# Kernel tuning notes

Hardware: AMD Instinct MI355X
Metric: run time of the kernel (lower is better)

Reference implementation:

```python
import jax, jax.numpy as jnp
import numpy as np

B, T, Rn, D, O, E, H, C, TM = 20, 20, 20, 4096, 16, 512, 8, 68, 1900


def l2norm(x, axis=-1, eps=1e-12):
    return x / jnp.maximum(jnp.linalg.norm(x, axis=axis, keepdims=True), eps)


def setup_inputs() -> dict:
    key = jax.random.key(0)
    ks = jax.random.split(key, 10)
    return {
        "features": jax.random.normal(ks[0], (B, T, Rn, D), jnp.float32),
        "labels": jax.random.randint(ks[1], (B, O), 0, C),
        "temporal_mem": jax.random.normal(ks[2], (TM, T, D), jnp.float32),
        "entity_W": jax.random.normal(ks[3], (C, E), jnp.float32) / np.float32(np.sqrt(C)),
        "entity_b": jnp.zeros((E,), jnp.float32),
        "Wq": jax.random.normal(ks[4], (E, E), jnp.float32) / np.float32(np.sqrt(E)),
        "Wk": jax.random.normal(ks[5], (D, E), jnp.float32) / np.float32(np.sqrt(D)),
        "Wv": jax.random.normal(ks[6], (D, E), jnp.float32) / np.float32(np.sqrt(D)),
        "Wo": jax.random.normal(ks[7], (E, E), jnp.float32) / np.float32(np.sqrt(E)),
        "obj_W1": jax.random.normal(ks[8], (D, E), jnp.float32) / np.float32(np.sqrt(D)),
        "obj_b1": jnp.zeros((E,), jnp.float32),
        "obj_W2": jax.random.normal(ks[9], (E, 1), jnp.float32) / np.float32(np.sqrt(E)),
        "obj_b2": jnp.zeros((1,), jnp.float32),
    }


def reference(features, labels, temporal_mem, entity_W, entity_b, Wq, Wk, Wv, Wo,
              obj_W1, obj_b1, obj_W2, obj_b2):
    beta = 0.5   # loss mixing weight (module's beta)
    qgce = 0.7   # generalized-CE exponent
    Dh = E // H
    # region features, L2-normalized (dataset_feat == 'CVPR' path)
    Rf = l2norm(features)                                   # [B,T,Rn,D]

    # ---- temporal memory-bank kNN retrieval ----
    R_max = l2norm(jnp.max(Rf, axis=2))                     # [B,T,D] max-pool over regions
    mem_max = l2norm(jnp.max(temporal_mem, axis=1))         # [TM,D] max-pool over frames
    sim = jnp.einsum('btd,md->btm', R_max, mem_max)         # [B,T,TM]
    idx = jnp.argmax(sim, axis=-1)                          # [B,T] nearest memory slot
    Rp = temporal_mem[idx]                                  # [B,T,T,D] gathered memory videos
    mem_feat = jnp.max(Rp, axis=2)                          # [B,T,D]

    # ---- entity (object-label) embedding: one-hot with class 0 zeroed ----
    onehot = jax.nn.one_hot(labels, C, dtype=features.dtype)
    onehot = onehot * (labels != 0)[..., None].astype(features.dtype)
    Qe = onehot @ entity_W + entity_b                       # [B,O,E]

    # ---- multi-head attention fusion over regions + retrieved memory ----
    kv = jnp.concatenate([Rf.reshape(B, T * Rn, D), mem_feat], axis=1)  # [B,N,D]
    q = (Qe @ Wq).reshape(B, O, H, Dh)
    k = (kv @ Wk).reshape(B, -1, H, Dh)
    v = (kv @ Wv).reshape(B, -1, H, Dh)
    scores = jnp.einsum('bohd,bnhd->bhon', q, k) / np.float32(np.sqrt(Dh))
    attn = jax.nn.softmax(scores, axis=-1)
    fused = jnp.einsum('bhon,bnhd->bohd', attn, v).reshape(B, O, E) @ Wo  # [B,O,E]

    # ---- top-k region objectness selection + generalized CE ----
    QR = jax.lax.stop_gradient(jnp.mean(scores, axis=1)[:, :, :T * Rn].reshape(B, O, T, Rn))
    hi = jnp.argmax(QR, axis=-1)                            # [B,O,T] top-1 region
    lo = jnp.argmin(QR, axis=-1)                            # [B,O,T] low region
    bidx = jnp.arange(B)[:, None, None]
    tidx = jnp.arange(T)[None, None, :]
    R_high = Rf[bidx, tidx, hi]                             # [B,O,T,D]
    R_low = Rf[bidx, tidx, lo]                              # [B,O,T,D]
    osel = (labels != 0).astype(features.dtype)             # [B,O]
    onum = jnp.maximum(jnp.sum(osel, axis=1), 1.0)
    mlp = lambda x: jax.nn.sigmoid(jnp.tanh(x @ obj_W1 + obj_b1) @ obj_W2 + obj_b2)
    s_hi = mlp(R_high * osel[..., None, None]).squeeze(-1)  # [B,O,T]
    s_lo = mlp(R_low * osel[..., None, None]).squeeze(-1)
    gce_hi = jnp.mean((1.0 - (s_hi + 1e-7) ** qgce) / qgce * osel[..., None], axis=-1)
    gce_lo = jnp.mean((1.0 - (1.0 - s_lo + 1e-7) ** qgce) / qgce * osel[..., None], axis=-1)
    gce = jnp.mean(jnp.sum(gce_hi, axis=1) / onum) + jnp.mean(jnp.sum(gce_lo, axis=1) / onum)

    return fused + beta * gce
```

## Files before the change

kernel.cpp:

```cpp
#include <hip/hip_runtime.h>

#define B_   20
#define T_   20
#define RN   20
#define D_   4096
#define O_   16
#define E_   512
#define H_   8
#define DH   64
#define TM_  1900
#define MREG 8192
#define NW   1536
#define NSIM 2048
#define MSIM 512
#define CAP  256
#define NT32 128

using f32x4  = __attribute__((ext_vector_type(4))) float;
using bf16x8 = __attribute__((ext_vector_type(8))) __bf16;

__device__ __forceinline__ unsigned short f2bf(float f){
  unsigned u = __float_as_uint(f);
  u += 0x7fffu + ((u >> 16) & 1u);
  return (unsigned short)(u >> 16);
}

__device__ __forceinline__ void st_bf4(unsigned short* dst, float4 v){
  ushort4 o = make_ushort4(f2bf(v.x), f2bf(v.y), f2bf(v.z), f2bf(v.w));
  *(ushort4*)dst = o;
}

__device__ __forceinline__ float bsum256(float v, float* sh){
  int t = threadIdx.x;
  for (int o = 32; o; o >>= 1) v += __shfl_down(v, o, 64);
  __syncthreads();
  if ((t & 63) == 0) sh[t >> 6] = v;
  __syncthreads();
  return sh[0] + sh[1] + sh[2] + sh[3];
}

__device__ __forceinline__ float bmax256(float v, float* sh){
  int t = threadIdx.x;
  for (int o = 32; o; o >>= 1) v = fmaxf(v, __shfl_down(v, o, 64));
  __syncthreads();
  if ((t & 63) == 0) sh[t >> 6] = v;
  __syncthreads();
  return fmaxf(fmaxf(sh[0], sh[1]), fmaxf(sh[2], sh[3]));
}

__device__ __forceinline__ void gld16(const void* g, void* l){
  __builtin_amdgcn_global_load_lds(
      (const __attribute__((address_space(1))) unsigned int*)g,
      (__attribute__((address_space(3))) unsigned int*)l, 16, 0, 0);
}

__global__ __launch_bounds__(256) void k_pre(
    const float* __restrict__ F, const float* __restrict__ TMm,
    const float* __restrict__ Wk, const float* __restrict__ Wv, const float* __restrict__ W1,
    unsigned short* __restrict__ Wall,
    unsigned short* __restrict__ A, float* __restrict__ rmaxr, float* __restrict__ rmsum,
    unsigned short* __restrict__ ubf,
    float* __restrict__ umax, float* __restrict__ msum, unsigned short* __restrict__ wnorm,
    unsigned short* __restrict__ gbf,
    const int* __restrict__ labels, const float* __restrict__ entW, const float* __restrict__ entB,
    const float* __restrict__ Wq, float* __restrict__ q){
  __shared__ char smem[4352];
  int bid = blockIdx.x, t = threadIdx.x;
  if (bid < 2048){
    int m = bid;
    if (m >= TM_){
      int4 zz = make_int4(0,0,0,0);
      int4* r1 = (int4*)(wnorm + (size_t)m*D_);
      int4* r2 = (int4*)(gbf + (size_t)m*D_);
      r1[t] = zz; r1[t + 256] = zz;
      r2[t] = zz; r2[t + 256] = zz;
      return;
    }
    float* sh = (float*)smem;
    const float* base = TMm + (size_t)m*T_*D_;
    float4 mx[4];
#pragma unroll
    for (int i = 0; i < 4; ++i) mx[i] = make_float4(-1e30f,-1e30f,-1e30f,-1e30f);
    float4 va[2][4];
#pragma unroll
    for (int i = 0; i < 4; ++i) va[0][i] = *(const float4*)(base + i*1024 + t*4);
#pragma unroll
    for (int f = 0; f < T_; ++f){
      int c = f & 1;
      if (f + 1 < T_){
#pragma unroll
        for (int i = 0; i < 4; ++i)
          va[c^1][i] = *(const float4*)(base + (size_t)(f+1)*D_ + i*1024 + t*4);
      }
#pragma unroll
      for (int i = 0; i < 4; ++i){
        mx[i].x = fmaxf(mx[i].x, va[c][i].x); mx[i].y = fmaxf(mx[i].y, va[c][i].y);
        mx[i].z = fmaxf(mx[i].z, va[c][i].z); mx[i].w = fmaxf(mx[i].w, va[c][i].w);
      }
    }
    float s = 0.f;
#pragma unroll
    for (int i = 0; i < 4; ++i){
      *(float4*)(umax + (size_t)m*D_ + i*1024 + t*4) = mx[i];
      st_bf4(gbf + (size_t)m*D_ + i*1024 + t*4, mx[i]);
      s += mx[i].x*mx[i].x + mx[i].y*mx[i].y + mx[i].z*mx[i].z + mx[i].w*mx[i].w;
    }
    s = bsum256(s, sh);
    if (t == 0) msum[m] = s;
    float inv = 1.f / fmaxf(sqrtf(s), 1e-12f);
#pragma unroll
    for (int i = 0; i < 4; ++i){
      float4 u = mx[i];
      u.x *= inv; u.y *= inv; u.z *= inv; u.w *= inv;
      st_bf4(wnorm + (size_t)m*D_ + i*1024 + t*4, u);
    }
  } else if (bid < 2560){
    int bt = bid - 2048;
    if (bt >= 400){
      int4 zz = make_int4(0,0,0,0);
      int4* r1 = (int4*)(ubf + (size_t)bt*D_);
      r1[t] = zz; r1[t + 256] = zz;
      int base = 8000 + (bt - 400)*2;
#pragma unroll
      for (int k = 0; k < 2; ++k){
        if (base + k < MREG){
          int4* r2 = (int4*)(A + (size_t)(base + k)*D_);
          r2[t] = zz; r2[t + 256] = zz;
        }
      }
      return;
    }
    float* sh = (float*)smem;
    const float* fb = F + (size_t)bt*RN*D_;
    unsigned short* ab = A + (size_t)bt*RN*D_;
    float4 mx[4];
#pragma unroll
    for (int i = 0; i < 4; ++i) mx[i] = make_float4(-1e30f,-1e30f,-1e30f,-1e30f);
    float4 vn[4];
#pragma unroll
    for (int i = 0; i < 4; ++i) vn[i] = *(const float4*)(fb + i*1024 + t*4);
    for (int r = 0; r < RN; ++r){
      float4 v[4];
      float s = 0.f;
#pragma unroll
      for (int i = 0; i < 4; ++i){
        v[i] = vn[i];
        s += v[i].x*v[i].x + v[i].y*v[i].y + v[i].z*v[i].z + v[i].w*v[i].w;
      }
      if (r + 1 < RN){
#pragma unroll
        for (int i = 0; i < 4; ++i)
          vn[i] = *(const float4*)(fb + (size_t)(r+1)*D_ + i*1024 + t*4);
      }
      s = bsum256(s, sh);
      float ri = 1.f / fmaxf(sqrtf(s), 1e-12f);
#pragma unroll
      for (int i = 0; i < 4; ++i){
        v[i].x *= ri; v[i].y *= ri; v[i].z *= ri; v[i].w *= ri;
        st_bf4(ab + (size_t)r*D_ + i*1024 + t*4, v[i]);
        mx[i].x = fmaxf(mx[i].x, v[i].x); mx[i].y = fmaxf(mx[i].y, v[i].y);
        mx[i].z = fmaxf(mx[i].z, v[i].z); mx[i].w = fmaxf(mx[i].w, v[i].w);
      }
    }
    float s2 = 0.f;
#pragma unroll
    for (int i = 0; i < 4; ++i){
      *(float4*)(rmaxr + (size_t)bt*D_ + i*1024 + t*4) = mx[i];
      s2 += mx[i].x*mx[i].x + mx[i].y*mx[i].y + mx[i].z*mx[i].z + mx[i].w*mx[i].w;
    }
    s2 = bsum256(s2, sh);
    if (t == 0) rmsum[bt] = s2;
    float inv = 1.f / fmaxf(sqrtf(s2), 1e-12f);
#pragma unroll
    for (int i = 0; i < 4; ++i){
      float4 u = mx[i];
      u.x *= inv; u.y *= inv; u.z *= inv; u.w *= inv;
      st_bf4(ubf + (size_t)bt*D_ + i*1024 + t*4, u);
    }
  } else if (bid < 8704){
    int wti = bid - 2560;
    float* tile = (float*)smem;
    int kb = (wti & 127) * 32, nb = (wti >> 7) * 32;
    const float* src; int nc0;
    if (nb < 512)      { src = Wk; nc0 = nb; }
    else if (nb < 1024){ src = Wv; nc0 = nb - 512; }
    else               { src = W1; nc0 = nb - 1024; }
    int tx = t & 31, ty = t >> 5;
#pragma unroll
    for (int j = 0; j < 4; ++j){
      int k = kb + ty + j*8;
      tile[(ty + j*8)*33 + tx] = src[(size_t)k*E_ + nc0 + tx];
    }
    __syncthreads();
#pragma unroll
    for (int j = 0; j < 4; ++j){
      int n = nb + ty + j*8;
      int k = kb + tx;
      Wall[(size_t)n*D_ + k] = f2bf(tile[tx*33 + ty + j*8]);
    }
  } else {
    int bo = bid - 8704;
    float* qe = (float*)smem;
    int lab = labels[bo];
    float sel = (lab != 0) ? 1.f : 0.f;
    qe[t]       = sel * entW[(size_t)lab*E_ + t]       + entB[t];
    qe[t + 256] = sel * entW[(size_t)lab*E_ + t + 256] + entB[t + 256];
    __syncthreads();
    float a0 = 0.f, a1 = 0.f;
    for (int ep = 0; ep < E_; ++ep){
      float r = qe[ep];
      a0 += r * Wq[(size_t)ep*E_ + t];
      a1 += r * Wq[(size_t)ep*E_ + t + 256];
    }
    q[(size_t)bo*E_ + t] = a0;
    q[(size_t)bo*E_ + t + 256] = a1;
  }
}

__global__ __launch_bounds__(512, 1) void k_gemm3(
    const unsigned short* __restrict__ Akv, const unsigned short* __restrict__ Wall,
    const unsigned short* __restrict__ ubf, const unsigned short* __restrict__ wnorm,
    const unsigned short* __restrict__ gbf,
    float* __restrict__ C2, float* __restrict__ simc, float* __restrict__ Gc){
  __shared__ char lds[98304];
  int bid = blockIdx.x;
  bid = (bid & 7)*32 + (bid >> 3);
  const unsigned short *A, *Bw; float* C; int nNt, ldc, mt, nt;
  if (bid < 192){       A = Akv; Bw = Wall;  C = C2;   nNt = 6; ldc = NW;   mt = bid/6;  nt = bid%6; }
  else if (bid < 208){  int s = bid - 192;
                        A = ubf; Bw = wnorm; C = simc; nNt = 8; ldc = NSIM; mt = s/8;    nt = s%8; }
  else {                int s = bid - 208;
                        A = gbf; Bw = Wall;  C = Gc;   nNt = 6; ldc = NW;   mt = s/6;    nt = s%6; }
  int tid = threadIdx.x, wid = tid >> 6, l = tid & 63;
  int wr = (wid >> 2) * 128;
  int wc = (wid & 3) * 64;
  int fr = l & 15, fq = l >> 4;
  const char* Ab = (const char*)A + (size_t)mt*256*(size_t)(D_*2);
  const char* Bb = (const char*)Bw + (size_t)nt*256*(size_t)(D_*2);
  f32x4 acc[8][4];
#pragma unroll
  for (int m = 0; m < 8; ++m)
#pragma unroll
    for (int n = 0; n < 4; ++n) acc[m][n] = (f32x4){0.f,0.f,0.f,0.f};

  auto stage = [&](char* dst, int ktt){
    int ktoff = ktt * 64;
#pragma unroll
    for (int i = 0; i < 2; ++i){
      int s = i*512 + tid;
      int row = s >> 2, u = s & 3;
      int ul = u ^ (row & 3);
      gld16(Ab + (size_t)row*(D_*2) + ktoff + ul*16, dst + s*16);
      gld16(Bb + (size_t)row*(D_*2) + ktoff + ul*16, dst + 16384 + s*16);
    }
  };

  stage(lds, 0);
  stage(lds + 32768, 1);
  stage(lds + 65536, 2);

  int cur = 0;
  for (int kt = 0; kt < NT32; ++kt){
    if (kt < NT32 - 2)       asm volatile("s_waitcnt vmcnt(8)" ::: "memory");
    else if (kt == NT32 - 2) asm volatile("s_waitcnt vmcnt(4)" ::: "memory");
    else                     asm volatile("s_waitcnt vmcnt(0)" ::: "memory");
    __builtin_amdgcn_s_barrier();
    __builtin_amdgcn_sched_barrier(0);
    const char* LA = lds + cur*32768;
    const char* LB = LA + 16384;
    bf16x8 bv[4];
#pragma unroll
    for (int n = 0; n < 4; ++n){
      int row = wc + n*16 + fr;
      int u = fq ^ (row & 3);
      bv[n] = *(const bf16x8*)(LB + row*64 + u*16);
    }
    __builtin_amdgcn_s_setprio(1);
#pragma unroll
    for (int mp = 0; mp < 4; ++mp){
      bf16x8 av[2];
#pragma unroll
      for (int mm = 0; mm < 2; ++mm){
        int row = wr + (mp*2 + mm)*16 + fr;
        int u = fq ^ (row & 3);
        av[mm] = *(const bf16x8*)(LA + row*64 + u*16);
      }
#pragma unroll
      for (int mm = 0; mm < 2; ++mm)
#pragma unroll
        for (int n = 0; n < 4; ++n)
          acc[mp*2 + mm][n] = __builtin_amdgcn_mfma_f32_16x16x32_bf16(
              av[mm], bv[n], acc[mp*2 + mm][n], 0, 0, 0);
    }
    __builtin_amdgcn_s_setprio(0);
    __builtin_amdgcn_s_barrier();
    if (kt + 3 < NT32)
      stage(lds + cur*32768, kt + 3);
    cur = (cur == 2) ? 0 : cur + 1;
  }
  size_t crow0 = (size_t)mt*256 + wr, ccol0 = (size_t)nt*256 + wc;
#pragma unroll
  for (int m = 0; m < 8; ++m)
#pragma unroll
    for (int n = 0; n < 4; ++n){
      size_t r0 = crow0 + m*16 + fq*4, c0 = ccol0 + n*16 + fr;
#pragma unroll
      for (int j = 0; j < 4; ++j)
        C[(r0 + j)*(size_t)ldc + c0] = acc[m][n][j];
    }
}

__global__ __launch_bounds__(256) void k_pick(const float* __restrict__ simc,
                                              const float* __restrict__ rmaxr, const float* __restrict__ rmsum,
                                              const float* __restrict__ umax, const float* __restrict__ msum,
                                              const float* __restrict__ Gc, float* __restrict__ C2){
  int bt = blockIdx.x, t = threadIdx.x;
  __shared__ float srow[1920];
  __shared__ float sh[4];
  __shared__ int cnt;
  __shared__ int cl[CAP];
  for (int m = t; m < TM_; m += 256) srow[m] = simc[(size_t)bt*NSIM + m];
  if (t == 0) cnt = 0;
  __syncthreads();
  float mx = -1e30f;
  for (int m = t; m < TM_; m += 256) mx = fmaxf(mx, srow[m]);
  mx = bmax256(mx, sh);
  float thr = mx - 2.5e-4f;
  for (int m = t; m < TM_; m += 256){
    if (srow[m] >= thr){
      int p = atomicAdd(&cnt, 1);
      if (p < CAP) cl[p] = m;
    }
  }
  __syncthreads();
  int cn = cnt < CAP ? cnt : CAP;
  float rinvv = 1.f / fmaxf(sqrtf(rmsum[bt]), 1e-12f);
  const float* a = rmaxr + (size_t)bt*D_;
  float best = -1e30f; int bestm = 0x7fffffff;
  for (int ci = 0; ci < cn; ++ci){
    int m = cl[ci];
    const float* wrow = umax + (size_t)m*D_;
    float p = 0.f;
    for (int i = t*4; i < D_; i += 1024){
      float4 av = *(const float4*)(a + i);
      float4 wv = *(const float4*)(wrow + i);
      p += av.x*wv.x + av.y*wv.y + av.z*wv.z + av.w*wv.w;
    }
    p = bsum256(p, sh);
    float sim = p * rinvv * (1.f / fmaxf(sqrtf(msum[m]), 1e-12f));
    if (sim > best || (sim == best && m < bestm)){ best = sim; bestm = m; }
  }
  const float4* src = (const float4*)(Gc + (size_t)bestm*NW);
  float4* dst = (float4*)(C2 + (size_t)(MREG + bt)*NW);
  if (t < 128){ dst[t] = src[t]; dst[t + 128] = src[t + 128]; dst[t + 256] = src[t + 256]; }
}

__global__ __launch_bounds__(256) void k_post(const float* __restrict__ q, const float* __restrict__ c2,
                                              float* __restrict__ fpre, int* __restrict__ hi,
                                              int* __restrict__ lo, const float* __restrict__ b1,
                                              const float* __restrict__ W2, const float* __restrict__ b2,
                                              float* __restrict__ z){
  __shared__ char smem[58368];
  int bid = blockIdx.x, t = threadIdx.x;
  if (bid < 160){
    int b = bid >> 3, h = bid & 7;
    int w = t >> 6, l = t & 63;
    float* qhp = (float*)smem;
    float* kb  = (float*)(smem + 4160);
    float* sc  = (float*)(smem + 31460);
    for (int i = t; i < O_*DH; i += 256){
      int o = i >> 6, d = i & 63;
      qhp[o*65 + d] = q[((size_t)(b*O_ + o))*E_ + h*DH + d] * 0.125f;
    }
    __syncthreads();
    for (int c = 0; c < 4; ++c){
      for (int i = t; i < 105*DH; i += 256){
        int j = i >> 6, d = i & 63;
        int n = c*105 + j;
        size_t row = n < 400 ? (size_t)b*400 + n : (size_t)MREG + b*20 + (n - 400);
        kb[j*65 + d] = c2[row*NW + h*DH + d];
      }
      __syncthreads();
      for (int i = t; i < O_*105; i += 256){
        int o = i / 105, j = i % 105;
        float acc = 0.f;
        for (int d = 0; d < DH; ++d) acc += qhp[o*65 + d] * kb[j*65 + d];
        sc[o*420 + c*105 + j] = acc;
      }
      __syncthreads();
    }
    for (int oi = 0; oi < 4; ++oi){
      int o = w + oi*4;
      float mxv = -1e30f;
      for (int n = l; n < 420; n += 64) mxv = fmaxf(mxv, sc[o*420 + n]);
      for (int of = 32; of; of >>= 1) mxv = fmaxf(mxv, __shfl_xor(mxv, of, 64));
      float sum = 0.f;
      for (int n = l; n < 420; n += 64){ float e = expf(sc[o*420 + n] - mxv); sc[o*420 + n] = e; sum += e; }
      for (int of = 32; of; of >>= 1) sum += __shfl_xor(sum, of, 64);
      float inv = 1.f / sum;
      for (int n = l; n < 420; n += 64) sc[o*420 + n] *= inv;
    }
    __syncthreads();
    float acc[4] = {0.f, 0.f, 0.f, 0.f};
    for (int c = 0; c < 4; ++c){
      for (int i = t; i < 105*DH; i += 256){
        int j = i >> 6, d = i & 63;
        int n = c*105 + j;
        size_t row = n < 400 ? (size_t)b*400 + n : (size_t)MREG + b*20 + (n - 400);
        kb[j*65 + d] = c2[row*NW + E_ + h*DH + d];
      }
      __syncthreads();
#pragma unroll
      for (int og = 0; og < 4; ++og){
        int o = og*4 + w;
        float a = 0.f;
        for (int j = 0; j < 105; ++j) a += sc[o*420 + c*105 + j] * kb[j*65 + l];
        acc[og] += a;
      }
      __syncthreads();
    }
#pragma unroll
    for (int og = 0; og < 4; ++og){
      int o = og*4 + w;
      fpre[((size_t)(b*O_ + o))*E_ + h*DH + l] = acc[og];
    }
  } else if (bid < 560){
    int bt = bid - 160;
    int b = bt / T_, tt = bt % T_;
    float* kl = (float*)smem;
    float* qr = (float*)(smem + 41040);
    for (int i = t; i < RN*E_; i += 256){
      int r = i >> 9, e = i & 511;
      kl[r*513 + e] = c2[((size_t)b*400 + tt*RN + r)*NW + e];
    }
    __syncthreads();
#pragma unroll
    for (int pp = 0; pp < 2; ++pp){
      int p = t + pp*256;
      if (p < O_*RN){
        int o = p / RN, r = p % RN;
        const float* qrow = q + ((size_t)(b*O_ + o))*E_;
        float acc = 0.f;
        for (int e = 0; e < E_; ++e) acc += qrow[e] * kl[r*513 + e];
        qr[o*20 + r] = acc;
      }
    }
    __syncthreads();
    if (t < O_){
      int o = t;
      float bh = qr[o*20], bl = qr[o*20]; int ih = 0, il = 0;
#pragma unroll
      for (int r = 1; r < RN; ++r){
        float v = qr[o*20 + r];
        if (v > bh){ bh = v; ih = r; }
        if (v < bl){ bl = v; il = r; }
      }
      int rowbase = b*400 + tt*RN;
      int outi = (b*O_ + o)*T_ + tt;
      hi[outi] = rowbase + ih;
      lo[outi] = rowbase + il;
    }
  } else {
    int g = (bid - 560)*4 + (t >> 6);
    int l = t & 63;
    const float* hrow = c2 + (size_t)g*NW + 1024;
    float acc = 0.f;
    for (int e = l; e < E_; e += 64) acc += tanhf(hrow[e] + b1[e]) * W2[e];
    for (int of = 32; of; of >>= 1) acc += __shfl_down(acc, of, 64);
    if (l == 0) z[g] = 1.f / (1.f + expf(-(acc + b2[0])));
  }
}

__global__ __launch_bounds__(256) void k_outg(const float* __restrict__ fpre, const float* __restrict__ Wo,
                                              const float* __restrict__ z, const int* __restrict__ hi,
                                              const int* __restrict__ lo, const int* __restrict__ labels,
                                              float* __restrict__ out){
  int bo = blockIdx.x, t = threadIdx.x;
  __shared__ float rowv[E_];
  __shared__ float vb[B_];
  __shared__ int cb[B_];
  __shared__ float gsh;
  rowv[t] = fpre[(size_t)bo*E_ + t];
  rowv[t + 256] = fpre[(size_t)bo*E_ + t + 256];
  if (t < B_){ vb[t] = 0.f; cb[t] = 0; }
  __syncthreads();
  for (int p = t; p < B_*O_; p += 256){
    int b = p / O_;
    if (labels[p] != 0){
      float acc = 0.f;
      for (int tt = 0; tt < T_; ++tt){
        float shi = z[hi[p*T_ + tt]];
        float slo = z[lo[p*T_ + tt]];
        acc += (1.f - __powf(shi + 1e-7f, 0.7f)) / 0.7f;
        acc += (1.f - __powf(1.f - slo + 1e-7f, 0.7f)) / 0.7f;
      }
      atomicAdd(&vb[b], acc / (float)T_);
      atomicAdd(&cb[b], 1);
    }
  }
  __syncthreads();
  if (t == 0){
    float g = 0.f;
    for (int b = 0; b < B_; ++b) g += vb[b] / fmaxf((float)cb[b], 1.f);
    gsh = 0.5f * (g / (float)B_);
  }
  __syncthreads();
  float g = gsh;
  float a0 = 0.f, a1 = 0.f;
  for (int ep = 0; ep < E_; ++ep){
    float r = rowv[ep];
    a0 += r * Wo[(size_t)ep*E_ + t];
    a1 += r * Wo[(size_t)ep*E_ + t + 256];
  }
  out[(size_t)bo*E_ + t] = a0 + g;
  out[(size_t)bo*E_ + t + 256] = a1 + g;
}

extern "C" void kernel_launch(void* const* d_in, const int* in_sizes, int n_in,
                              void* d_out, int out_size, void* d_ws, size_t ws_size,
                              hipStream_t stream) {
  (void)in_sizes; (void)n_in; (void)out_size; (void)ws_size;
  const float* F    = (const float*)d_in[0];
  const int*   labels = (const int*)d_in[1];
  const float* TMm  = (const float*)d_in[2];
  const float* entW = (const float*)d_in[3];
  const float* entB = (const float*)d_in[4];
  const float* Wq   = (const float*)d_in[5];
  const float* Wk   = (const float*)d_in[6];
  const float* Wv   = (const float*)d_in[7];
  const float* Wo   = (const float*)d_in[8];
  const float* W1   = (const float*)d_in[9];
  const float* b1   = (const float*)d_in[10];
  const float* W2   = (const float*)d_in[11];
  const float* b2   = (const float*)d_in[12];
  float* out = (float*)d_out;

  size_t off = 0;
  char* wsb = (char*)d_ws;
  auto alloc = [&](size_t bytes) -> char* {
    char* p = wsb + off; off += (bytes + 255) & ~(size_t)255; return p;
  };
  unsigned short* A_kv = (unsigned short*)alloc((size_t)MREG * D_ * 2);
  unsigned short* Wall = (unsigned short*)alloc((size_t)NW * D_ * 2);
  float* umax          = (float*)alloc((size_t)TM_ * D_ * 4);
  unsigned short* gbf  = (unsigned short*)alloc((size_t)NSIM * D_ * 2);
  unsigned short* wnorm= (unsigned short*)alloc((size_t)NSIM * D_ * 2);
  unsigned short* ubf  = (unsigned short*)alloc((size_t)MSIM * D_ * 2);
  float* rmaxr = (float*)alloc((size_t)400 * D_ * 4);
  float* simc  = (float*)alloc((size_t)MSIM * NSIM * 4);
  float* Gc    = (float*)alloc((size_t)NSIM * NW * 4);
  float* C2    = (float*)alloc((size_t)(MREG + 512) * NW * 4);
  float* qbuf  = (float*)alloc((size_t)B_ * O_ * E_ * 4);
  float* fpre  = (float*)alloc((size_t)B_ * O_ * E_ * 4);
  float* rmsum = (float*)alloc(400 * 4);
  float* msum  = (float*)alloc(TM_ * 4);
  int*   hib   = (int*)alloc(6400 * 4);
  int*   lob   = (int*)alloc(6400 * 4);
  float* zbuf  = (float*)alloc(8000 * 4);

  k_pre<<<9024, 256, 0, stream>>>(F, TMm, Wk, Wv, W1, Wall, A_kv, rmaxr, rmsum, ubf,
                                  umax, msum, wnorm, gbf, labels, entW, entB, Wq, qbuf);
  k_gemm3<<<256, 512, 0, stream>>>(A_kv, Wall, ubf, wnorm, gbf, C2, simc, Gc);
  k_pick<<<400, 256, 0, stream>>>(simc, rmaxr, rmsum, umax, msum, Gc, C2);
  k_post<<<2560, 256, 0, stream>>>(qbuf, C2, fpre, hib, lob, b1, W2, b2, zbuf);
  k_outg<<<B_*O_, 256, 0, stream>>>(fpre, Wo, zbuf, hib, lob, labels, out);
}
```

Baseline: 514.7 us.

## Shrink GEMM tiles to 128x128 with single-buffered LDS and more blocks

```diff
diff --git a/kernel.cpp b/kernel.cpp
--- a/kernel.cpp
+++ b/kernel.cpp
@@ -14,7 +14,6 @@
 #define NSIM 2048
 #define MSIM 512
 #define CAP  256
-#define NT32 128
 
 using f32x4  = __attribute__((ext_vector_type(4))) float;
 using bf16x8 = __attribute__((ext_vector_type(8))) __bf16;
@@ -217,93 +216,70 @@
   }
 }
 
-__global__ __launch_bounds__(512, 1) void k_gemm3(
+__global__ __launch_bounds__(256, 2) void k_gemm3(
     const unsigned short* __restrict__ Akv, const unsigned short* __restrict__ Wall,
     const unsigned short* __restrict__ ubf, const unsigned short* __restrict__ wnorm,
     const unsigned short* __restrict__ gbf,
     float* __restrict__ C2, float* __restrict__ simc, float* __restrict__ Gc){
-  __shared__ char lds[98304];
+  __shared__ char lds[32768];
   int bid = blockIdx.x;
-  bid = (bid & 7)*32 + (bid >> 3);
+  bid = (bid & 7)*128 + (bid >> 3);
   const unsigned short *A, *Bw; float* C; int nNt, ldc, mt, nt;
-  if (bid < 192){       A = Akv; Bw = Wall;  C = C2;   nNt = 6; ldc = NW;   mt = bid/6;  nt = bid%6; }
-  else if (bid < 208){  int s = bid - 192;
-                        A = ubf; Bw = wnorm; C = simc; nNt = 8; ldc = NSIM; mt = s/8;    nt = s%8; }
-  else {                int s = bid - 208;
-                        A = gbf; Bw = Wall;  C = Gc;   nNt = 6; ldc = NW;   mt = s/6;    nt = s%6; }
-  int tid = threadIdx.x, wid = tid >> 6, l = tid & 63;
-  int wr = (wid >> 2) * 128;
-  int wc = (wid & 3) * 64;
-  int fr = l & 15, fq = l >> 4;
-  const char* Ab = (const char*)A + (size_t)mt*256*(size_t)(D_*2);
-  const char* Bb = (const char*)Bw + (size_t)nt*256*(size_t)(D_*2);
-  f32x4 acc[8][4];
-#pragma unroll
-  for (int m = 0; m < 8; ++m)
+  if (bid < 768){       A = Akv; Bw = Wall;  C = C2;   nNt = 12; ldc = NW;   mt = bid/12;     nt = bid%12; }
+  else if (bid < 832){  int s = bid - 768;
+                        A = ubf; Bw = wnorm; C = simc; nNt = 16; ldc = NSIM; mt = s/16;       nt = s%16; }
+  else {                int s = bid - 832;
+                        A = gbf; Bw = Wall;  C = Gc;   nNt = 12; ldc = NW;   mt = s/12;       nt = s%12; }
+  int tid = threadIdx.x, wv = tid >> 6, l = tid & 63;
+  int wr = (wv >> 1) * 64, wc = (wv & 1) * 64;
+  const char* Ab = (const char*)A + (size_t)mt*128*(size_t)(D_*2);
+  const char* Bb = (const char*)Bw + (size_t)nt*128*(size_t)(D_*2);
+  f32x4 acc[4][4];
+#pragma unroll
+  for (int m = 0; m < 4; ++m)
 #pragma unroll
     for (int n = 0; n < 4; ++n) acc[m][n] = (f32x4){0.f,0.f,0.f,0.f};
-
-  auto stage = [&](char* dst, int ktt){
-    int ktoff = ktt * 64;
-#pragma unroll
-    for (int i = 0; i < 2; ++i){
-      int s = i*512 + tid;
-      int row = s >> 2, u = s & 3;
-      int ul = u ^ (row & 3);
-      gld16(Ab + (size_t)row*(D_*2) + ktoff + ul*16, dst + s*16);
-      gld16(Bb + (size_t)row*(D_*2) + ktoff + ul*16, dst + 16384 + s*16);
-    }
-  };
-
-  stage(lds, 0);
-  stage(lds + 32768, 1);
-  stage(lds + 65536, 2);
-
-  int cur = 0;
-  for (int kt = 0; kt < NT32; ++kt){
-    if (kt < NT32 - 2)       asm volatile("s_waitcnt vmcnt(8)" ::: "memory");
-    else if (kt == NT32 - 2) asm volatile("s_waitcnt vmcnt(4)" ::: "memory");
-    else                     asm volatile("s_waitcnt vmcnt(0)" ::: "memory");
-    __builtin_amdgcn_s_barrier();
-    __builtin_amdgcn_sched_barrier(0);
-    const char* LA = lds + cur*32768;
-    const char* LB = LA + 16384;
-    bf16x8 bv[4];
+  for (int kt = 0; kt < D_/64; ++kt){
+    int ktoff = kt*128;
+#pragma unroll
+    for (int i = 0; i < 4; ++i){
+      int idx = i*256 + tid;
+      int row = idx >> 3, u = idx & 7;
+      int ul = u ^ (row & 7);
+      gld16(Ab + (size_t)row*(D_*2) + ktoff + ul*16, lds + i*4096 + wv*1024);
+      gld16(Bb + (size_t)row*(D_*2) + ktoff + ul*16, lds + 16384 + i*4096 + wv*1024);
+    }
+    __syncthreads();
+#pragma unroll
+    for (int kk = 0; kk < 2; ++kk){
+      bf16x8 av[4], bv[4];
+#pragma unroll
+      for (int m = 0; m < 4; ++m){
+        int row = wr + m*16 + (l & 15);
+        int u = (kk*4 + (l >> 4)) ^ (row & 7);
+        av[m] = *(const bf16x8*)(lds + row*128 + u*16);
+      }
+#pragma unroll
+      for (int n = 0; n < 4; ++n){
+        int row = wc + n*16 + (l & 15);
+        int u = (kk*4 + (l >> 4)) ^ (row & 7);
+        bv[n] = *(const bf16x8*)(lds + 16384 + row*128 + u*16);
+      }
+#pragma unroll
+      for (int m = 0; m < 4; ++m)
+#pragma unroll
+        for (int n = 0; n < 4; ++n)
+          acc[m][n] = __builtin_amdgcn_mfma_f32_16x16x32_bf16(av[m], bv[n], acc[m][n], 0, 0, 0);
+    }
+    __syncthreads();
+  }
+  int rq = (l >> 4) * 4, cq = l & 15;
+  size_t crow0 = (size_t)mt*128 + wr, ccol0 = (size_t)nt*128 + wc;
+#pragma unroll
+  for (int m = 0; m < 4; ++m)
 #pragma unroll
     for (int n = 0; n < 4; ++n){
-      int row = wc + n*16 + fr;
-      int u = fq ^ (row & 3);
-      bv[n] = *(const bf16x8*)(LB + row*64 + u*16);
-    }
-    __builtin_amdgcn_s_setprio(1);
-#pragma unroll
-    for (int mp = 0; mp < 4; ++mp){
-      bf16x8 av[2];
-#pragma unroll
-      for (int mm = 0; mm < 2; ++mm){
-        int row = wr + (mp*2 + mm)*16 + fr;
-        int u = fq ^ (row & 3);
-        av[mm] = *(const bf16x8*)(LA + row*64 + u*16);
-      }
-#pragma unroll
-      for (int mm = 0; mm < 2; ++mm)
-#pragma unroll
-        for (int n = 0; n < 4; ++n)
-          acc[mp*2 + mm][n] = __builtin_amdgcn_mfma_f32_16x16x32_bf16(
-              av[mm], bv[n], acc[mp*2 + mm][n], 0, 0, 0);
-    }
-    __builtin_amdgcn_s_setprio(0);
-    __builtin_amdgcn_s_barrier();
-    if (kt + 3 < NT32)
-      stage(lds + cur*32768, kt + 3);
-    cur = (cur == 2) ? 0 : cur + 1;
-  }
-  size_t crow0 = (size_t)mt*256 + wr, ccol0 = (size_t)nt*256 + wc;
-#pragma unroll
-  for (int m = 0; m < 8; ++m)
-#pragma unroll
-    for (int n = 0; n < 4; ++n){
-      size_t r0 = crow0 + m*16 + fq*4, c0 = ccol0 + n*16 + fr;
+      size_t r0 = crow0 + m*16 + rq, c0 = ccol0 + n*16 + cq;
 #pragma unroll
       for (int j = 0; j < 4; ++j)
         C[(r0 + j)*(size_t)ldc + c0] = acc[m][n][j];
@@ -560,7 +536,7 @@
 
   k_pre<<<9024, 256, 0, stream>>>(F, TMm, Wk, Wv, W1, Wall, A_kv, rmaxr, rmsum, ubf,
                                   umax, msum, wnorm, gbf, labels, entW, entB, Wq, qbuf);
-  k_gemm3<<<256, 512, 0, stream>>>(A_kv, Wall, ubf, wnorm, gbf, C2, simc, Gc);
+  k_gemm3<<<1024, 256, 0, stream>>>(A_kv, Wall, ubf, wnorm, gbf, C2, simc, Gc);
   k_pick<<<400, 256, 0, stream>>>(simc, rmaxr, rmsum, umax, msum, Gc, C2);
   k_post<<<2560, 256, 0, stream>>>(qbuf, C2, fpre, hib, lob, b1, W2, b2, zbuf);
   k_outg<<<B_*O_, 256, 0, stream>>>(fpre, Wo, zbuf, hib, lob, labels, out);
```

After: 518.7 us. About the same (+0.8%).
